# Kernel optimization log

Hardware: AMD Instinct MI355X
Metric: run time of the kernel (lower is better)

The kernel has to match this reference:

```python
import jax, jax.numpy as jnp
import numpy as np

N_NODES = 100000
N_REL = 3
N_EDGES = 300000
IN_FEAT = 256
OUT_FEAT = 256


def setup_inputs() -> dict:
    key = jax.random.key(0)
    k1, k2, k3, k4 = jax.random.split(key, 4)
    x = jax.random.normal(k1, (N_NODES, IN_FEAT), dtype=jnp.float32)
    weight = jax.random.normal(k2, (N_REL, IN_FEAT, OUT_FEAT), dtype=jnp.float32)
    src = jax.random.randint(k3, (N_REL, N_EDGES), 0, N_NODES, dtype=jnp.int64)
    dst = jax.random.randint(k4, (N_REL, N_EDGES), 0, N_NODES, dtype=jnp.int64)
    return {"x": x, "weight": weight, "src": src, "dst": dst}


def reference(x, weight, src, dst):
    # Per-relation dense transform: h[r] = x @ W[r]   -> [R, N, out]
    h = jnp.einsum('ni,rio->rno', x, weight)
    n_nodes = x.shape[0]

    # Sparse unweighted-sum aggregation per relation (adj @ h), accumulated
    # into a single destination-node buffer (single node type).
    def agg_one(h_r, src_r, dst_r):
        msgs = h_r[src_r]  # gather source features [E, out]
        return jax.ops.segment_sum(msgs, dst_r, num_segments=n_nodes)

    per_rel = jax.vmap(agg_one)(h, src, dst)  # [R, N, out]
    return jax.nn.relu(per_rel.sum(axis=0))
```

## Files before the change

kernel.cpp:

```cpp
#include <hip/hip_runtime.h>
#include <hip/hip_bf16.h>
#include <stdint.h>

#define M_NODES 100000
#define KF 256
#define NF 256
#define NRELS 3
#define NEDGES 300000
#define TOT_EDGES (NRELS * NEDGES)
#define TOTK (NRELS * M_NODES)
#define KCAT (NRELS * KF)
#define BM 64
#define PAD 32
#define XELEM (M_NODES * KF)
#define EB ((TOT_EDGES + 255) / 256)
#define XCONV_BLOCKS (XELEM / 8 / 256)
#define WT_BLOCKS ((NF * KCAT + 255) / 256)

typedef __attribute__((ext_vector_type(8))) short bf16x8;
typedef __attribute__((ext_vector_type(8))) unsigned short u16x8;
typedef __attribute__((ext_vector_type(4))) float f32x4;

__device__ __forceinline__ unsigned short f32_to_bf16(float f) {
    union { float f; uint32_t u; } c; c.f = f;
    uint32_t u = c.u;
    uint32_t r = (u + 0x7FFFu + ((u >> 16) & 1u)) >> 16;
    return (unsigned short)r;
}

__device__ __forceinline__ float bf16_to_f32(unsigned short s) {
    union { uint32_t u; float f; } c; c.u = ((uint32_t)s) << 16;
    return c.f;
}

__global__ __launch_bounds__(256)
void k_build(const float* __restrict__ x, const float* __restrict__ w,
             const int* __restrict__ src, const int* __restrict__ dst,
             unsigned short* __restrict__ xb, unsigned short* __restrict__ Bt,
             int* __restrict__ counts, int* __restrict__ perm)
{
    int b = blockIdx.x;
    if (b < EB) {
        int e = b * 256 + threadIdx.x;
        if (e < TOT_EDGES) {
            int r = e / NEDGES;
            int key = r * M_NODES + dst[e];
            int pos = atomicAdd(&counts[key], 1);
            if (pos < PAD)
                perm[(size_t)key * PAD + pos] = src[e];
        }
    } else if (b < EB + XCONV_BLOCKS) {
        int gid = (b - EB) * 256 + threadIdx.x;
        const float4* p = (const float4*)x + (size_t)gid * 2;
        float4 u = p[0], v = p[1];
        u16x8 o;
        o[0] = f32_to_bf16(u.x); o[1] = f32_to_bf16(u.y);
        o[2] = f32_to_bf16(u.z); o[3] = f32_to_bf16(u.w);
        o[4] = f32_to_bf16(v.x); o[5] = f32_to_bf16(v.y);
        o[6] = f32_to_bf16(v.z); o[7] = f32_to_bf16(v.w);
        *(u16x8*)(xb + (size_t)gid * 8) = o;
    } else {
        int gid = (b - EB - XCONV_BLOCKS) * 256 + threadIdx.x;
        if (gid < NF * KCAT) {
            int n = gid / KCAT;
            int kc = gid - n * KCAT;
            int r = kc >> 8, k = kc & 255;
            Bt[(size_t)n * KCAT + kc] = f32_to_bf16(w[((size_t)r * KF + k) * NF + n]);
        }
    }
}

__global__ __launch_bounds__(256, 4)
void gemm_ga(const unsigned short* __restrict__ xb,
             const unsigned short* __restrict__ Bt,
             const int* __restrict__ cnt, const int* __restrict__ perm,
             float* __restrict__ out)
{
    const int d0 = blockIdx.x * BM;
    const int t = threadIdx.x;
    const int lane = t & 63;
    const int wc = t >> 6;
    const int l16 = lane & 15, lg = lane >> 4;
    const int hw = t >> 5;
    const int hl = t & 31;

    __shared__ short As[BM * 256];

    f32x4 acc[4][4] = {};
    const u16x8 zz = (u16x8)0;

    int oc0 = 0, oc1 = 0, oc2 = 0;
    if (hl < 8) {
        int kb = d0 + hw * 8 + hl;
        if (kb >= M_NODES) kb = M_NODES - 1;
        oc0 = cnt[kb];
        oc1 = cnt[M_NODES + kb];
        oc2 = cnt[2 * M_NODES + kb];
    }

    for (int r = 0; r < NRELS; ++r) {
        if (r) __syncthreads();
        int ocr = (r == 0) ? oc0 : ((r == 1) ? oc1 : oc2);

        int pv[8];
#pragma unroll
        for (int q = 0; q < 8; ++q) {
            int kq = d0 + hw * 8 + q;
            if (kq >= M_NODES) kq = M_NODES - 1;
            pv[q] = perm[((size_t)(r * M_NODES + kq)) * PAD + hl];
        }

#pragma unroll
        for (int q = 0; q < 8; ++q) {
            int n = __shfl(ocr, q, 32);
            if (n > PAD) n = PAD;
            float a0=0.f,a1=0.f,a2=0.f,a3=0.f,a4=0.f,a5=0.f,a6=0.f,a7=0.f;
            for (int j = 0; j < n; j += 4) {
                int s0 = __shfl(pv[q], j + 0, 32);
                int s1 = __shfl(pv[q], j + 1, 32);
                int s2 = __shfl(pv[q], j + 2, 32);
                int s3 = __shfl(pv[q], j + 3, 32);
                u16x8 v0 = *(const u16x8*)(xb + (size_t)s0 * KF + hl * 8);
                u16x8 v1 = (j + 1 < n) ? *(const u16x8*)(xb + (size_t)s1 * KF + hl * 8) : zz;
                u16x8 v2 = (j + 2 < n) ? *(const u16x8*)(xb + (size_t)s2 * KF + hl * 8) : zz;
                u16x8 v3 = (j + 3 < n) ? *(const u16x8*)(xb + (size_t)s3 * KF + hl * 8) : zz;
                a0 += bf16_to_f32(v0[0]) + bf16_to_f32(v1[0]) + bf16_to_f32(v2[0]) + bf16_to_f32(v3[0]);
                a1 += bf16_to_f32(v0[1]) + bf16_to_f32(v1[1]) + bf16_to_f32(v2[1]) + bf16_to_f32(v3[1]);
                a2 += bf16_to_f32(v0[2]) + bf16_to_f32(v1[2]) + bf16_to_f32(v2[2]) + bf16_to_f32(v3[2]);
                a3 += bf16_to_f32(v0[3]) + bf16_to_f32(v1[3]) + bf16_to_f32(v2[3]) + bf16_to_f32(v3[3]);
                a4 += bf16_to_f32(v0[4]) + bf16_to_f32(v1[4]) + bf16_to_f32(v2[4]) + bf16_to_f32(v3[4]);
                a5 += bf16_to_f32(v0[5]) + bf16_to_f32(v1[5]) + bf16_to_f32(v2[5]) + bf16_to_f32(v3[5]);
                a6 += bf16_to_f32(v0[6]) + bf16_to_f32(v1[6]) + bf16_to_f32(v2[6]) + bf16_to_f32(v3[6]);
                a7 += bf16_to_f32(v0[7]) + bf16_to_f32(v1[7]) + bf16_to_f32(v2[7]) + bf16_to_f32(v3[7]);
            }
            int row = hw * 8 + q;
            u16x8 o;
            o[0] = f32_to_bf16(a0); o[1] = f32_to_bf16(a1);
            o[2] = f32_to_bf16(a2); o[3] = f32_to_bf16(a3);
            o[4] = f32_to_bf16(a4); o[5] = f32_to_bf16(a5);
            o[6] = f32_to_bf16(a6); o[7] = f32_to_bf16(a7);
            int slot = hl ^ (row & 7);
            *(u16x8*)((char*)As + row * 512 + slot * 16) = o;
        }
        __syncthreads();

        const unsigned short* bb = Bt + (size_t)(wc * 64 + l16) * KCAT
                                      + r * 256 + lg * 8;
        for (int kt = 0; kt < 8; ++kt) {
            bf16x8 b[4];
#pragma unroll
            for (int j = 0; j < 4; ++j)
                b[j] = *(const bf16x8*)(bb + (size_t)j * 16 * KCAT + kt * 32);
            bf16x8 a[4];
#pragma unroll
            for (int i = 0; i < 4; ++i) {
                int arow = i * 16 + l16;
                int slot = (kt * 4 + lg) ^ (arow & 7);
                a[i] = *(bf16x8*)((char*)As + arow * 512 + slot * 16);
            }
#pragma unroll
            for (int i = 0; i < 4; ++i)
#pragma unroll
                for (int j = 0; j < 4; ++j)
                    acc[i][j] = __builtin_amdgcn_mfma_f32_16x16x32_bf16(
                        a[i], b[j], acc[i][j], 0, 0, 0);
        }
    }

#pragma unroll
    for (int i = 0; i < 4; ++i) {
        int row_base = d0 + i * 16 + lg * 4;
#pragma unroll
        for (int q = 0; q < 4; ++q) {
            int row = row_base + q;
            if (row < M_NODES) {
#pragma unroll
                for (int j = 0; j < 4; ++j) {
                    int col = wc * 64 + j * 16 + l16;
                    out[(size_t)row * NF + col] = fmaxf(acc[i][j][q], 0.f);
                }
            }
        }
    }
}

extern "C" void kernel_launch(void* const* d_in, const int* in_sizes, int n_in,
                              void* d_out, int out_size, void* d_ws, size_t ws_size,
                              hipStream_t stream)
{
    const float* x   = (const float*)d_in[0];
    const float* w   = (const float*)d_in[1];
    const int*   src = (const int*)d_in[2];
    const int*   dst = (const int*)d_in[3];
    float* out = (float*)d_out;

    char* ws = (char*)d_ws;
    size_t o = 0;
    int* counts = (int*)(ws + o);  o += (size_t)TOTK * 4;
    int* perm   = (int*)(ws + o);  o += (size_t)TOTK * PAD * 4;
    unsigned short* Bt = (unsigned short*)(ws + o); o += (size_t)NF * KCAT * 2;
    unsigned short* xb = (unsigned short*)(ws + o); o += (size_t)XELEM * 2;

    hipMemsetAsync(counts, 0, (size_t)TOTK * 4, stream);

    k_build<<<EB + XCONV_BLOCKS + WT_BLOCKS, 256, 0, stream>>>(
        x, w, src, dst, xb, Bt, counts, perm);

    gemm_ga<<<(M_NODES + BM - 1) / BM, 256, 0, stream>>>(
        xb, Bt, counts, perm, out);
}
```

Measured before the change: 260.7 us.

## Halve row tile to 32 and prefetch only first 8 neighbor indices per row

Shrinks the block row tile from 64 to 32 nodes, producing twice as many blocks and raising the occupancy hint to 5 blocks per CU. Each half-warp now prefetches the first 8 source indices for 4 rows in one load and fetches the overflow indices only when a row has more than 8 edges. Counts for all three relations are loaded in one go and broadcast by shuffle. The intent is better latency hiding and fewer wasted perm loads, given the mean in-degree of about 3. The cost is that each block re-reads the full B matrix for only 32 rows, doubling B traffic per output row.

```diff
diff --git a/kernel.cpp b/kernel.cpp
--- a/kernel.cpp
+++ b/kernel.cpp
@@ -10,7 +10,7 @@
 #define TOT_EDGES (NRELS * NEDGES)
 #define TOTK (NRELS * M_NODES)
 #define KCAT (NRELS * KF)
-#define BM 64
+#define BM 32
 #define PAD 32
 #define XELEM (M_NODES * KF)
 #define EB ((TOT_EDGES + 255) / 256)
@@ -70,7 +70,7 @@
     }
 }
 
-__global__ __launch_bounds__(256, 4)
+__global__ __launch_bounds__(256, 5)
 void gemm_ga(const unsigned short* __restrict__ xb,
              const unsigned short* __restrict__ Bt,
              const int* __restrict__ cnt, const int* __restrict__ perm,
@@ -86,44 +86,41 @@
 
     __shared__ short As[BM * 256];
 
-    f32x4 acc[4][4] = {};
+    f32x4 acc[2][4] = {};
     const u16x8 zz = (u16x8)0;
 
-    int oc0 = 0, oc1 = 0, oc2 = 0;
-    if (hl < 8) {
-        int kb = d0 + hw * 8 + hl;
+    int oc = 0;
+    if (hl < 12) {
+        int kb = d0 + hw * 4 + (hl & 3);
         if (kb >= M_NODES) kb = M_NODES - 1;
-        oc0 = cnt[kb];
-        oc1 = cnt[M_NODES + kb];
-        oc2 = cnt[2 * M_NODES + kb];
+        oc = cnt[(hl >> 2) * M_NODES + kb];
     }
 
     for (int r = 0; r < NRELS; ++r) {
         if (r) __syncthreads();
-        int ocr = (r == 0) ? oc0 : ((r == 1) ? oc1 : oc2);
-
-        int pv[8];
-#pragma unroll
-        for (int q = 0; q < 8; ++q) {
-            int kq = d0 + hw * 8 + q;
+
+        int kpre = d0 + hw * 4 + (hl >> 3);
+        if (kpre >= M_NODES) kpre = M_NODES - 1;
+        int pv = perm[((size_t)(r * M_NODES + kpre)) * PAD + (hl & 7)];
+
+#pragma unroll
+        for (int q = 0; q < 4; ++q) {
+            int n = __shfl(oc, r * 4 + q, 32);
+            if (n > PAD) n = PAD;
+            int kq = d0 + hw * 4 + q;
             if (kq >= M_NODES) kq = M_NODES - 1;
-            pv[q] = perm[((size_t)(r * M_NODES + kq)) * PAD + hl];
-        }
-
-#pragma unroll
-        for (int q = 0; q < 8; ++q) {
-            int n = __shfl(ocr, q, 32);
-            if (n > PAD) n = PAD;
             float a0=0.f,a1=0.f,a2=0.f,a3=0.f,a4=0.f,a5=0.f,a6=0.f,a7=0.f;
-            for (int j = 0; j < n; j += 4) {
-                int s0 = __shfl(pv[q], j + 0, 32);
-                int s1 = __shfl(pv[q], j + 1, 32);
-                int s2 = __shfl(pv[q], j + 2, 32);
-                int s3 = __shfl(pv[q], j + 3, 32);
+
+            int n8 = (n < 8) ? n : 8;
+            for (int j = 0; j < n8; j += 4) {
+                int s0 = __shfl(pv, q * 8 + j + 0, 32);
+                int s1 = __shfl(pv, q * 8 + j + 1, 32);
+                int s2 = __shfl(pv, q * 8 + j + 2, 32);
+                int s3 = __shfl(pv, q * 8 + j + 3, 32);
                 u16x8 v0 = *(const u16x8*)(xb + (size_t)s0 * KF + hl * 8);
-                u16x8 v1 = (j + 1 < n) ? *(const u16x8*)(xb + (size_t)s1 * KF + hl * 8) : zz;
-                u16x8 v2 = (j + 2 < n) ? *(const u16x8*)(xb + (size_t)s2 * KF + hl * 8) : zz;
-                u16x8 v3 = (j + 3 < n) ? *(const u16x8*)(xb + (size_t)s3 * KF + hl * 8) : zz;
+                u16x8 v1 = (j + 1 < n8) ? *(const u16x8*)(xb + (size_t)s1 * KF + hl * 8) : zz;
+                u16x8 v2 = (j + 2 < n8) ? *(const u16x8*)(xb + (size_t)s2 * KF + hl * 8) : zz;
+                u16x8 v3 = (j + 3 < n8) ? *(const u16x8*)(xb + (size_t)s3 * KF + hl * 8) : zz;
                 a0 += bf16_to_f32(v0[0]) + bf16_to_f32(v1[0]) + bf16_to_f32(v2[0]) + bf16_to_f32(v3[0]);
                 a1 += bf16_to_f32(v0[1]) + bf16_to_f32(v1[1]) + bf16_to_f32(v2[1]) + bf16_to_f32(v3[1]);
                 a2 += bf16_to_f32(v0[2]) + bf16_to_f32(v1[2]) + bf16_to_f32(v2[2]) + bf16_to_f32(v3[2]);
@@ -133,7 +130,29 @@
                 a6 += bf16_to_f32(v0[6]) + bf16_to_f32(v1[6]) + bf16_to_f32(v2[6]) + bf16_to_f32(v3[6]);
                 a7 += bf16_to_f32(v0[7]) + bf16_to_f32(v1[7]) + bf16_to_f32(v2[7]) + bf16_to_f32(v3[7]);
             }
-            int row = hw * 8 + q;
+            if (n > 8) {
+                int ex = (hl < n - 8) ? perm[((size_t)(r * M_NODES + kq)) * PAD + 8 + hl] : 0;
+                for (int j = 8; j < n; j += 4) {
+                    int s0 = __shfl(ex, j - 8 + 0, 32);
+                    int s1 = __shfl(ex, j - 8 + 1, 32);
+                    int s2 = __shfl(ex, j - 8 + 2, 32);
+                    int s3 = __shfl(ex, j - 8 + 3, 32);
+                    u16x8 v0 = *(const u16x8*)(xb + (size_t)s0 * KF + hl * 8);
+                    u16x8 v1 = (j + 1 < n) ? *(const u16x8*)(xb + (size_t)s1 * KF + hl * 8) : zz;
+                    u16x8 v2 = (j + 2 < n) ? *(const u16x8*)(xb + (size_t)s2 * KF + hl * 8) : zz;
+                    u16x8 v3 = (j + 3 < n) ? *(const u16x8*)(xb + (size_t)s3 * KF + hl * 8) : zz;
+                    a0 += bf16_to_f32(v0[0]) + bf16_to_f32(v1[0]) + bf16_to_f32(v2[0]) + bf16_to_f32(v3[0]);
+                    a1 += bf16_to_f32(v0[1]) + bf16_to_f32(v1[1]) + bf16_to_f32(v2[1]) + bf16_to_f32(v3[1]);
+                    a2 += bf16_to_f32(v0[2]) + bf16_to_f32(v1[2]) + bf16_to_f32(v2[2]) + bf16_to_f32(v3[2]);
+                    a3 += bf16_to_f32(v0[3]) + bf16_to_f32(v1[3]) + bf16_to_f32(v2[3]) + bf16_to_f32(v3[3]);
+                    a4 += bf16_to_f32(v0[4]) + bf16_to_f32(v1[4]) + bf16_to_f32(v2[4]) + bf16_to_f32(v3[4]);
+                    a5 += bf16_to_f32(v0[5]) + bf16_to_f32(v1[5]) + bf16_to_f32(v2[5]) + bf16_to_f32(v3[5]);
+                    a6 += bf16_to_f32(v0[6]) + bf16_to_f32(v1[6]) + bf16_to_f32(v2[6]) + bf16_to_f32(v3[6]);
+                    a7 += bf16_to_f32(v0[7]) + bf16_to_f32(v1[7]) + bf16_to_f32(v2[7]) + bf16_to_f32(v3[7]);
+                }
+            }
+
+            int row = hw * 4 + q;
             u16x8 o;
             o[0] = f32_to_bf16(a0); o[1] = f32_to_bf16(a1);
             o[2] = f32_to_bf16(a2); o[3] = f32_to_bf16(a3);
@@ -151,15 +170,15 @@
 #pragma unroll
             for (int j = 0; j < 4; ++j)
                 b[j] = *(const bf16x8*)(bb + (size_t)j * 16 * KCAT + kt * 32);
-            bf16x8 a[4];
-#pragma unroll
-            for (int i = 0; i < 4; ++i) {
+            bf16x8 a[2];
+#pragma unroll
+            for (int i = 0; i < 2; ++i) {
                 int arow = i * 16 + l16;
                 int slot = (kt * 4 + lg) ^ (arow & 7);
                 a[i] = *(bf16x8*)((char*)As + arow * 512 + slot * 16);
             }
 #pragma unroll
-            for (int i = 0; i < 4; ++i)
+            for (int i = 0; i < 2; ++i)
 #pragma unroll
                 for (int j = 0; j < 4; ++j)
                     acc[i][j] = __builtin_amdgcn_mfma_f32_16x16x32_bf16(
@@ -168,7 +187,7 @@
     }
 
 #pragma unroll
-    for (int i = 0; i < 4; ++i) {
+    for (int i = 0; i < 2; ++i) {
         int row_base = d0 + i * 16 + lg * 4;
 #pragma unroll
         for (int q = 0; q < 4; ++q) {
```

After: 265.1 us. Within noise of the previous version (+1.7%).

## Restructure neighbor gather to batch loads for two rows and prefetch perm

Applied to the files above, without the earlier changes.

The gather phase now loads the first eight neighbor indices for all eight rows with two coalesced perm reads per lane, issued before the barrier. It processes two destination rows at a time so up to eight independent row gathers are in flight, with a slow path for rows that have more than eight neighbors. The MFMA k-loop is fully unrolled. The aim is more memory-level parallelism and less latency in the irregular gather, at the cost of more registers and code size.

```diff
diff --git a/kernel.cpp b/kernel.cpp
--- a/kernel.cpp
+++ b/kernel.cpp
@@ -98,72 +98,140 @@
         oc2 = cnt[2 * M_NODES + kb];
     }
 
+    int kpre = d0 + hw * 8 + (hl >> 2);
+    if (kpre >= M_NODES) kpre = M_NODES - 1;
+
     for (int r = 0; r < NRELS; ++r) {
+        int ocr = (r == 0) ? oc0 : ((r == 1) ? oc1 : oc2);
+
+        size_t pbase = ((size_t)(r * M_NODES + kpre)) * PAD + (hl & 3);
+        int pv0 = perm[pbase];
+        int pv1 = perm[pbase + 4];
+
         if (r) __syncthreads();
-        int ocr = (r == 0) ? oc0 : ((r == 1) ? oc1 : oc2);
-
-        int pv[8];
-#pragma unroll
-        for (int q = 0; q < 8; ++q) {
-            int kq = d0 + hw * 8 + q;
-            if (kq >= M_NODES) kq = M_NODES - 1;
-            pv[q] = perm[((size_t)(r * M_NODES + kq)) * PAD + hl];
-        }
-
-#pragma unroll
-        for (int q = 0; q < 8; ++q) {
-            int n = __shfl(ocr, q, 32);
-            if (n > PAD) n = PAD;
-            float a0=0.f,a1=0.f,a2=0.f,a3=0.f,a4=0.f,a5=0.f,a6=0.f,a7=0.f;
-            for (int j = 0; j < n; j += 4) {
-                int s0 = __shfl(pv[q], j + 0, 32);
-                int s1 = __shfl(pv[q], j + 1, 32);
-                int s2 = __shfl(pv[q], j + 2, 32);
-                int s3 = __shfl(pv[q], j + 3, 32);
-                u16x8 v0 = *(const u16x8*)(xb + (size_t)s0 * KF + hl * 8);
-                u16x8 v1 = (j + 1 < n) ? *(const u16x8*)(xb + (size_t)s1 * KF + hl * 8) : zz;
-                u16x8 v2 = (j + 2 < n) ? *(const u16x8*)(xb + (size_t)s2 * KF + hl * 8) : zz;
-                u16x8 v3 = (j + 3 < n) ? *(const u16x8*)(xb + (size_t)s3 * KF + hl * 8) : zz;
-                a0 += bf16_to_f32(v0[0]) + bf16_to_f32(v1[0]) + bf16_to_f32(v2[0]) + bf16_to_f32(v3[0]);
-                a1 += bf16_to_f32(v0[1]) + bf16_to_f32(v1[1]) + bf16_to_f32(v2[1]) + bf16_to_f32(v3[1]);
-                a2 += bf16_to_f32(v0[2]) + bf16_to_f32(v1[2]) + bf16_to_f32(v2[2]) + bf16_to_f32(v3[2]);
-                a3 += bf16_to_f32(v0[3]) + bf16_to_f32(v1[3]) + bf16_to_f32(v2[3]) + bf16_to_f32(v3[3]);
-                a4 += bf16_to_f32(v0[4]) + bf16_to_f32(v1[4]) + bf16_to_f32(v2[4]) + bf16_to_f32(v3[4]);
-                a5 += bf16_to_f32(v0[5]) + bf16_to_f32(v1[5]) + bf16_to_f32(v2[5]) + bf16_to_f32(v3[5]);
-                a6 += bf16_to_f32(v0[6]) + bf16_to_f32(v1[6]) + bf16_to_f32(v2[6]) + bf16_to_f32(v3[6]);
-                a7 += bf16_to_f32(v0[7]) + bf16_to_f32(v1[7]) + bf16_to_f32(v2[7]) + bf16_to_f32(v3[7]);
-            }
-            int row = hw * 8 + q;
-            u16x8 o;
-            o[0] = f32_to_bf16(a0); o[1] = f32_to_bf16(a1);
-            o[2] = f32_to_bf16(a2); o[3] = f32_to_bf16(a3);
-            o[4] = f32_to_bf16(a4); o[5] = f32_to_bf16(a5);
-            o[6] = f32_to_bf16(a6); o[7] = f32_to_bf16(a7);
-            int slot = hl ^ (row & 7);
-            *(u16x8*)((char*)As + row * 512 + slot * 16) = o;
+
+        auto LD = [&](int pv, int idx) -> u16x8 {
+            int s = __shfl(pv, idx, 32);
+            return *(const u16x8*)(xb + (size_t)s * KF + hl * 8);
+        };
+
+#pragma unroll
+        for (int qp = 0; qp < 4; ++qp) {
+            const int q0 = qp * 2, q1 = q0 + 1;
+            int n0 = __shfl(ocr, q0, 32); if (n0 > PAD) n0 = PAD;
+            int n1 = __shfl(ocr, q1, 32); if (n1 > PAD) n1 = PAD;
+
+            u16x8 u0 = zz, u1 = zz, u2 = zz, u3 = zz;
+            u16x8 w0 = zz, w1 = zz, w2 = zz, w3 = zz;
+            if (n0 > 0) {
+                u0 = LD(pv0, q0 * 4 + 0);
+                if (n0 > 1) u1 = LD(pv0, q0 * 4 + 1);
+                if (n0 > 2) u2 = LD(pv0, q0 * 4 + 2);
+                if (n0 > 3) u3 = LD(pv0, q0 * 4 + 3);
+            }
+            if (n1 > 0) {
+                w0 = LD(pv0, q1 * 4 + 0);
+                if (n1 > 1) w1 = LD(pv0, q1 * 4 + 1);
+                if (n1 > 2) w2 = LD(pv0, q1 * 4 + 2);
+                if (n1 > 3) w3 = LD(pv0, q1 * 4 + 3);
+            }
+
+            float a[8] = {}, b[8] = {};
+#pragma unroll
+            for (int j = 0; j < 8; ++j)
+                a[j] = bf16_to_f32(u0[j]) + bf16_to_f32(u1[j])
+                     + bf16_to_f32(u2[j]) + bf16_to_f32(u3[j]);
+#pragma unroll
+            for (int j = 0; j < 8; ++j)
+                b[j] = bf16_to_f32(w0[j]) + bf16_to_f32(w1[j])
+                     + bf16_to_f32(w2[j]) + bf16_to_f32(w3[j]);
+
+            if (n0 > 4) {
+                u0 = LD(pv1, q0 * 4 + 0);
+                u1 = (n0 > 5) ? LD(pv1, q0 * 4 + 1) : zz;
+                u2 = (n0 > 6) ? LD(pv1, q0 * 4 + 2) : zz;
+                u3 = (n0 > 7) ? LD(pv1, q0 * 4 + 3) : zz;
+#pragma unroll
+                for (int j = 0; j < 8; ++j)
+                    a[j] += bf16_to_f32(u0[j]) + bf16_to_f32(u1[j])
+                          + bf16_to_f32(u2[j]) + bf16_to_f32(u3[j]);
+            }
+            if (n1 > 4) {
+                w0 = LD(pv1, q1 * 4 + 0);
+                w1 = (n1 > 5) ? LD(pv1, q1 * 4 + 1) : zz;
+                w2 = (n1 > 6) ? LD(pv1, q1 * 4 + 2) : zz;
+                w3 = (n1 > 7) ? LD(pv1, q1 * 4 + 3) : zz;
+#pragma unroll
+                for (int j = 0; j < 8; ++j)
+                    b[j] += bf16_to_f32(w0[j]) + bf16_to_f32(w1[j])
+                          + bf16_to_f32(w2[j]) + bf16_to_f32(w3[j]);
+            }
+
+            if (n0 > 8) {
+                int kq = d0 + hw * 8 + q0;
+                if (kq >= M_NODES) kq = M_NODES - 1;
+                int ex = (hl < n0 - 8)
+                    ? perm[((size_t)(r * M_NODES + kq)) * PAD + 8 + hl] : 0;
+                for (int j = 8; j < n0; ++j) {
+                    int s = __shfl(ex, j - 8, 32);
+                    u16x8 v = *(const u16x8*)(xb + (size_t)s * KF + hl * 8);
+#pragma unroll
+                    for (int m = 0; m < 8; ++m) a[m] += bf16_to_f32(v[m]);
+                }
+            }
+            if (n1 > 8) {
+                int kq = d0 + hw * 8 + q1;
+                if (kq >= M_NODES) kq = M_NODES - 1;
+                int ex = (hl < n1 - 8)
+                    ? perm[((size_t)(r * M_NODES + kq)) * PAD + 8 + hl] : 0;
+                for (int j = 8; j < n1; ++j) {
+                    int s = __shfl(ex, j - 8, 32);
+                    u16x8 v = *(const u16x8*)(xb + (size_t)s * KF + hl * 8);
+#pragma unroll
+                    for (int m = 0; m < 8; ++m) b[m] += bf16_to_f32(v[m]);
+                }
+            }
+
+            {
+                int row = hw * 8 + q0;
+                u16x8 o;
+#pragma unroll
+                for (int j = 0; j < 8; ++j) o[j] = f32_to_bf16(a[j]);
+                int slot = hl ^ (row & 7);
+                *(u16x8*)((char*)As + row * 512 + slot * 16) = o;
+            }
+            {
+                int row = hw * 8 + q1;
+                u16x8 o;
+#pragma unroll
+                for (int j = 0; j < 8; ++j) o[j] = f32_to_bf16(b[j]);
+                int slot = hl ^ (row & 7);
+                *(u16x8*)((char*)As + row * 512 + slot * 16) = o;
+            }
         }
         __syncthreads();
 
         const unsigned short* bb = Bt + (size_t)(wc * 64 + l16) * KCAT
                                       + r * 256 + lg * 8;
+#pragma unroll
         for (int kt = 0; kt < 8; ++kt) {
-            bf16x8 b[4];
+            bf16x8 bfr[4];
 #pragma unroll
             for (int j = 0; j < 4; ++j)
-                b[j] = *(const bf16x8*)(bb + (size_t)j * 16 * KCAT + kt * 32);
-            bf16x8 a[4];
+                bfr[j] = *(const bf16x8*)(bb + (size_t)j * 16 * KCAT + kt * 32);
+            bf16x8 afr[4];
 #pragma unroll
             for (int i = 0; i < 4; ++i) {
                 int arow = i * 16 + l16;
                 int slot = (kt * 4 + lg) ^ (arow & 7);
-                a[i] = *(bf16x8*)((char*)As + arow * 512 + slot * 16);
+                afr[i] = *(bf16x8*)((char*)As + arow * 512 + slot * 16);
             }
 #pragma unroll
             for (int i = 0; i < 4; ++i)
 #pragma unroll
                 for (int j = 0; j < 4; ++j)
                     acc[i][j] = __builtin_amdgcn_mfma_f32_16x16x32_bf16(
-                        a[i], b[j], acc[i][j], 0, 0, 0);
+                        afr[i], bfr[j], acc[i][j], 0, 0, 0);
         }
     }
 
```

Result: slower. 324.6 us (+24.5%).
